# Performance work log

Hardware: AMD Instinct MI355X
Metric: run time of the kernel (lower is better)

Reference implementation:

```python
import jax, jax.numpy as jnp
import numpy as np

N, IN_DIM, OUT_DIM, HEADS = 4096, 256, 256, 8
D_HEAD = (OUT_DIM * HEADS) // HEADS  # = OUT_DIM per the torch code
HIDDEN = OUT_DIM * 4
LN_EPS = 1e-5


def setup_inputs() -> dict:
    key = jax.random.key(0)
    ks = jax.random.split(key, 8)
    s = 0.02
    return {
        "x": jax.random.normal(ks[0], (N, IN_DIM), jnp.float32),
        "Wq": jax.random.normal(ks[1], (OUT_DIM * HEADS, IN_DIM), jnp.float32) * s,
        "Wk": jax.random.normal(ks[2], (OUT_DIM * HEADS, IN_DIM), jnp.float32) * s,
        "Wv": jax.random.normal(ks[3], (OUT_DIM * HEADS, IN_DIM), jnp.float32) * s,
        "Wo": jax.random.normal(ks[4], (OUT_DIM, OUT_DIM * HEADS), jnp.float32) * s,
        "bo": jnp.zeros((OUT_DIM,), jnp.float32),
        "ln1_g": jnp.ones((IN_DIM,), jnp.float32),
        "ln1_b": jnp.zeros((IN_DIM,), jnp.float32),
        "ln2_g": jnp.ones((OUT_DIM,), jnp.float32),
        "ln2_b": jnp.zeros((OUT_DIM,), jnp.float32),
        "W1": jax.random.normal(ks[5], (HIDDEN, OUT_DIM), jnp.float32) * s,
        "b1": jnp.zeros((HIDDEN,), jnp.float32),
        "W2": jax.random.normal(ks[6], (OUT_DIM, HIDDEN), jnp.float32) * s,
        "b2": jnp.zeros((OUT_DIM,), jnp.float32),
    }


def _layernorm(x, g, b):
    mu = jnp.mean(x, axis=-1, keepdims=True)
    var = jnp.mean(jnp.square(x - mu), axis=-1, keepdims=True)
    return (x - mu) * jax.lax.rsqrt(var + LN_EPS) * g + b


def reference(x, Wq, Wk, Wv, Wo, bo, ln1_g, ln1_b, ln2_g, ln2_b, W1, b1, W2, b2):
    n = x.shape[0]
    h = _layernorm(x, ln1_g, ln1_b)
    # projections: F.linear(h, W) = h @ W.T, viewed as [N, H, d_head]
    Q = (h @ Wq.T).reshape(n, HEADS, D_HEAD)
    K = (h @ Wk.T).reshape(n, HEADS, D_HEAD)
    V = (h @ Wv.T).reshape(n, HEADS, D_HEAD)
    scores = jnp.einsum('nhd,mhd->nhm', Q, K) / jnp.sqrt(jnp.float32(D_HEAD))
    probs = jax.nn.softmax(scores, axis=-1)
    attn = jnp.einsum('nhm,mhd->nhd', probs, V).reshape(n, HEADS * D_HEAD)
    attn_out = attn @ Wo.T + bo
    x = x + attn_out  # proj_residual is Identity (in_dim == out_dim)
    h2 = _layernorm(x, ln2_g, ln2_b)
    ffn = jax.nn.gelu(h2 @ W1.T + b1, approximate=False) @ W2.T + b2
    return x + ffn
```

## Files before the change

kernel.cpp:

```cpp
#include <hip/hip_runtime.h>

typedef __attribute__((ext_vector_type(8))) short short8;
typedef __attribute__((ext_vector_type(4))) float f32x4;
typedef __attribute__((ext_vector_type(16))) float f32x16;
typedef __attribute__((ext_vector_type(8))) int i32x8;
typedef unsigned short u16;
typedef unsigned int u32;
typedef unsigned char u8;

#define DEVFN static __device__ __forceinline__

DEVFN u16 f2b(float f) {
  u32 u = __builtin_bit_cast(u32, f);
  u32 r = u + 0x7fffu + ((u >> 16) & 1u);
  return (u16)(r >> 16);
}

DEVFN float b2f(u16 b) {
  u32 u = ((u32)b) << 16;
  return __builtin_bit_cast(float, u);
}

DEVFN short8 ldfrag(const void* p) {
  return __builtin_bit_cast(short8, *(const uint4*)p);
}

#define MFMA16(a, b, c) __builtin_amdgcn_mfma_f32_16x16x32_bf16((a), (b), (c), 0, 0, 0)
#define MFMAS(a, b, c) __builtin_amdgcn_mfma_scale_f32_32x32x64_f8f6f4((a), (b), (c), 0, 0, 0, 127, 0, 127)
#define EXP2(x) __builtin_amdgcn_exp2f(x)

DEVFN i32x8 mk8(uint4 a, uint4 b) {
  return (i32x8){(int)a.x, (int)a.y, (int)a.z, (int)a.w, (int)b.x, (int)b.y, (int)b.z, (int)b.w};
}

DEVFN void llds16(const void* g, void* l) {
  __builtin_amdgcn_global_load_lds((const __attribute__((address_space(1))) void*)g,
                                   (__attribute__((address_space(3))) void*)l, 16, 0, 0);
}

DEVFN float gelu_exact(float v) {
  return 0.5f * v * (1.0f + erff(v * 0.70710678118654752f));
}

DEVFN int sigma(int d) {
  return (d & ~24) | ((d & 8) << 1) | ((d & 16) >> 1);
}

__global__ __launch_bounds__(256) void k_prep(const float* s0, const float* s1, const float* s2,
                                              const float* s3, const float* s4, const float* s5,
                                              u16* d0, u16* d1, u16* d2, u16* d3, u16* d4, u16* d5,
                                              const float* x, const float* g1, const float* be1,
                                              u16* hb) {
  const int y = blockIdx.y;
  if (y < 6) {
    int i = blockIdx.x * 256 + threadIdx.x;
    const float* s;
    u16* d;
    int n4;
    switch (y) {
      case 0: s = s0; d = d0; n4 = 131072; break;
      case 1: s = s1; d = d1; n4 = 131072; break;
      case 2: s = s2; d = d2; n4 = 131072; break;
      case 3: s = s3; d = d3; n4 = 131072; break;
      case 4: s = s4; d = d4; n4 = 65536; break;
      default: s = s5; d = d5; n4 = 65536; break;
    }
    if (i >= n4) return;
    float4 v = ((const float4*)s)[i];
    ushort4 o = { f2b(v.x), f2b(v.y), f2b(v.z), f2b(v.w) };
    ((ushort4*)d)[i] = o;
    return;
  }
  int row = blockIdx.x * 4 + (threadIdx.x >> 6);
  int l = threadIdx.x & 63;
  const float4 v = *(const float4*)(x + (size_t)row * 256 + l * 4);
  float s = v.x + v.y + v.z + v.w;
#pragma unroll
  for (int m = 1; m < 64; m <<= 1) s += __shfl_xor(s, m);
  float mu = s * (1.0f / 256.0f);
  float dx = v.x - mu, dy = v.y - mu, dz = v.z - mu, dw = v.w - mu;
  float q = dx * dx + dy * dy + dz * dz + dw * dw;
#pragma unroll
  for (int m = 1; m < 64; m <<= 1) q += __shfl_xor(q, m);
  float r = rsqrtf(q * (1.0f / 256.0f) + 1e-5f);
  float4 gv = *(const float4*)(g1 + l * 4);
  float4 bv = *(const float4*)(be1 + l * 4);
  ushort4 o = { f2b(dx * r * gv.x + bv.x), f2b(dy * r * gv.y + bv.y),
                f2b(dz * r * gv.z + bv.z), f2b(dw * r * gv.w + bv.w) };
  *(ushort4*)(hb + (size_t)row * 256 + l * 4) = o;
}

template <int EPI>
__global__ __launch_bounds__(256, 2) void k_gemm(const u16* __restrict__ A,
                                                 const u16* __restrict__ B,
                                                 void* __restrict__ out,
                                                 const float* __restrict__ bias,
                                                 int M, int N, int K) {
  __shared__ __attribute__((aligned(16))) u16 As[128 * 32];
  __shared__ __attribute__((aligned(16))) u16 Bs[128 * 32];
  const int t = threadIdx.x;
  const int w = t >> 6, l = t & 63, g = l >> 4, c = l & 15;
  const int wr = w >> 1, wc = w & 1;
  const int bm = blockIdx.y, bn = blockIdx.x;

  f32x4 acc[4][4] = {};
  int nk = K >> 5, kk0 = 0;
  if (EPI == 4) { nk = nk / gridDim.z; kk0 = blockIdx.z * nk; }

  const int srow = t >> 2;
  const int sj = t & 3;
  const char* Abase = (const char*)A;
  const char* Bbase = (const char*)B;

  for (int kk = kk0; kk < kk0 + nk; ++kk) {
    const size_t kb = (size_t)kk * 64;
    uint4 a0 = *(const uint4*)(Abase + ((size_t)(bm * 128 + srow) * K) * 2 + kb + sj * 16);
    uint4 a1 = *(const uint4*)(Abase + ((size_t)(bm * 128 + srow + 64) * K) * 2 + kb + sj * 16);
    uint4 b0 = *(const uint4*)(Bbase + ((size_t)(bn * 128 + srow) * K) * 2 + kb + sj * 16);
    uint4 b1 = *(const uint4*)(Bbase + ((size_t)(bn * 128 + srow + 64) * K) * 2 + kb + sj * 16);
    __syncthreads();
    const int sw0 = (sj * 16) ^ (((srow >> 1) & 3) << 4);
    const int sw1 = (sj * 16) ^ ((((srow + 64) >> 1) & 3) << 4);
    *(uint4*)((char*)As + srow * 64 + sw0) = a0;
    *(uint4*)((char*)As + (srow + 64) * 64 + sw1) = a1;
    *(uint4*)((char*)Bs + srow * 64 + sw0) = b0;
    *(uint4*)((char*)Bs + (srow + 64) * 64 + sw1) = b1;
    __syncthreads();
    short8 af[4], bfr[4];
#pragma unroll
    for (int m = 0; m < 4; ++m) {
      int row = wr * 64 + m * 16 + c;
      af[m] = ldfrag((const char*)As + row * 64 + ((g * 16) ^ (((row >> 1) & 3) << 4)));
    }
#pragma unroll
    for (int n = 0; n < 4; ++n) {
      int row = wc * 64 + n * 16 + c;
      bfr[n] = ldfrag((const char*)Bs + row * 64 + ((g * 16) ^ (((row >> 1) & 3) << 4)));
    }
#pragma unroll
    for (int m = 0; m < 4; ++m)
#pragma unroll
      for (int n = 0; n < 4; ++n) acc[m][n] = MFMA16(af[m], bfr[n], acc[m][n]);
  }

  const int row0 = bm * 128 + wr * 64 + 4 * g;
  const int col0 = bn * 128 + wc * 64 + c;
#pragma unroll
  for (int m = 0; m < 4; ++m) {
#pragma unroll
    for (int n = 0; n < 4; ++n) {
      const int row = row0 + m * 16;
      const int col = col0 + n * 16;
      if (EPI == 3) {
        float bc = bias[col];
#pragma unroll
        for (int rr = 0; rr < 4; ++rr)
          ((u16*)out)[(size_t)(row + rr) * N + col] = f2b(gelu_exact(acc[m][n][rr] + bc));
      } else {
        float* po = (float*)out + (size_t)blockIdx.z * M * N;
#pragma unroll
        for (int rr = 0; rr < 4; ++rr)
          po[(size_t)(row + rr) * N + col] = acc[m][n][rr];
      }
    }
  }
}

__global__ __launch_bounds__(256, 2) void k_gemm_wo(const u16* __restrict__ part,
                                                    const float* __restrict__ ml,
                                                    const u16* __restrict__ B,
                                                    float* __restrict__ out) {
  constexpr int M = 4096, N = 256, K = 2048;
  __shared__ __attribute__((aligned(16))) u16 As[128 * 32];
  __shared__ __attribute__((aligned(16))) u16 Bs[128 * 32];
  const int t = threadIdx.x;
  const int w = t >> 6, l = t & 63, g = l >> 4, c = l & 15;
  const int wr = w >> 1, wc = w & 1;
  const int bm = blockIdx.y, bn = blockIdx.x;
  const int nk = 16, kk0 = blockIdx.z * 16;
  const int h0 = kk0 >> 3;

  const int srow = t >> 2;
  const int sj = t & 3;
  const int r0 = bm * 128 + srow, r1 = r0 + 64;

  float wgt[4];
#pragma unroll
  for (int rr = 0; rr < 2; ++rr) {
    const int row = rr ? r1 : r0;
#pragma unroll
    for (int hh = 0; hh < 2; ++hh) {
      const int h = h0 + hh;
      float l0 = ml[(0 + h) * 4096 + row];
      float l1 = ml[(8 + h) * 4096 + row];
      wgt[rr * 2 + hh] = 1.0f / (l0 + l1);
    }
  }

  f32x4 acc[4][4] = {};
  const char* Pbase = (const char*)part;
  const char* Bbase = (const char*)B;
  const size_t PSTRIDE = (size_t)4096 * 2048 * 2;

  for (int kk = kk0; kk < kk0 + nk; ++kk) {
    const int hh = (kk >> 3) & 1;
    const size_t kb = (size_t)kk * 64;
    const size_t a0off = ((size_t)r0 * K) * 2 + kb + sj * 16;
    const size_t a1off = ((size_t)r1 * K) * 2 + kb + sj * 16;
    uint4 p00 = *(const uint4*)(Pbase + a0off);
    uint4 p01 = *(const uint4*)(Pbase + PSTRIDE + a0off);
    uint4 p10 = *(const uint4*)(Pbase + a1off);
    uint4 p11 = *(const uint4*)(Pbase + PSTRIDE + a1off);
    uint4 b0 = *(const uint4*)(Bbase + ((size_t)(bn * 128 + srow) * K) * 2 + kb + sj * 16);
    uint4 b1 = *(const uint4*)(Bbase + ((size_t)(bn * 128 + srow + 64) * K) * 2 + kb + sj * 16);

    float w0 = wgt[hh], w1 = wgt[2 + hh];
    uint4 a0, a1;
    {
      const u16* x0 = (const u16*)&p00;
      const u16* x1 = (const u16*)&p01;
      u16* o = (u16*)&a0;
#pragma unroll
      for (int j = 0; j < 8; ++j) o[j] = f2b((b2f(x0[j]) + b2f(x1[j])) * w0);
      const u16* y0 = (const u16*)&p10;
      const u16* y1 = (const u16*)&p11;
      u16* o1 = (u16*)&a1;
#pragma unroll
      for (int j = 0; j < 8; ++j) o1[j] = f2b((b2f(y0[j]) + b2f(y1[j])) * w1);
    }

    __syncthreads();
    const int sw0 = (sj * 16) ^ (((srow >> 1) & 3) << 4);
    const int sw1 = (sj * 16) ^ ((((srow + 64) >> 1) & 3) << 4);
    *(uint4*)((char*)As + srow * 64 + sw0) = a0;
    *(uint4*)((char*)As + (srow + 64) * 64 + sw1) = a1;
    *(uint4*)((char*)Bs + srow * 64 + sw0) = b0;
    *(uint4*)((char*)Bs + (srow + 64) * 64 + sw1) = b1;
    __syncthreads();
    short8 af[4], bfr[4];
#pragma unroll
    for (int m = 0; m < 4; ++m) {
      int row = wr * 64 + m * 16 + c;
      af[m] = ldfrag((const char*)As + row * 64 + ((g * 16) ^ (((row >> 1) & 3) << 4)));
    }
#pragma unroll
    for (int n = 0; n < 4; ++n) {
      int row = wc * 64 + n * 16 + c;
      bfr[n] = ldfrag((const char*)Bs + row * 64 + ((g * 16) ^ (((row >> 1) & 3) << 4)));
    }
#pragma unroll
    for (int m = 0; m < 4; ++m)
#pragma unroll
      for (int n = 0; n < 4; ++n) acc[m][n] = MFMA16(af[m], bfr[n], acc[m][n]);
  }

  const int row0 = bm * 128 + wr * 64 + 4 * g;
  const int col0 = bn * 128 + wc * 64 + c;
  float* po = out + (size_t)blockIdx.z * M * N;
#pragma unroll
  for (int m = 0; m < 4; ++m)
#pragma unroll
    for (int n = 0; n < 4; ++n)
#pragma unroll
      for (int rr = 0; rr < 4; ++rr)
        po[(size_t)(row0 + m * 16 + rr) * N + col0 + n * 16] = acc[m][n][rr];
}

__global__ __launch_bounds__(256, 2) void k_gemm_qkv(const u16* __restrict__ A,
                                                     const u16* __restrict__ Bq,
                                                     const u16* __restrict__ Bk,
                                                     const u16* __restrict__ Bv,
                                                     u8* __restrict__ Oq,
                                                     u8* __restrict__ Ok,
                                                     u8* __restrict__ Ov8) {
  constexpr int M = 4096, N = 2048, K = 256;
  __shared__ __attribute__((aligned(16))) u16 As[128 * 32];
  __shared__ __attribute__((aligned(16))) u16 Bs[128 * 32];
  const int t = threadIdx.x;
  const int w = t >> 6, l = t & 63, g = l >> 4, c = l & 15;
  const int wr = w >> 1, wc = w & 1;
  const int sel = blockIdx.x >> 4;
  const int bn = blockIdx.x & 15;
  const int bm = blockIdx.y;
  const u16* B = sel == 0 ? Bq : (sel == 1 ? Bk : Bv);

  f32x4 acc[4][4] = {};
  const int srow = t >> 2;
  const int sj = t & 3;
  const char* Abase = (const char*)A;
  const char* Bbase = (const char*)B;

  for (int kk = 0; kk < 8; ++kk) {
    const size_t kb = (size_t)kk * 64;
    uint4 a0 = *(const uint4*)(Abase + ((size_t)(bm * 128 + srow) * K) * 2 + kb + sj * 16);
    uint4 a1 = *(const uint4*)(Abase + ((size_t)(bm * 128 + srow + 64) * K) * 2 + kb + sj * 16);
    uint4 b0 = *(const uint4*)(Bbase + ((size_t)(bn * 128 + srow) * K) * 2 + kb + sj * 16);
    uint4 b1 = *(const uint4*)(Bbase + ((size_t)(bn * 128 + srow + 64) * K) * 2 + kb + sj * 16);
    __syncthreads();
    const int sw0 = (sj * 16) ^ (((srow >> 1) & 3) << 4);
    const int sw1 = (sj * 16) ^ ((((srow + 64) >> 1) & 3) << 4);
    *(uint4*)((char*)As + srow * 64 + sw0) = a0;
    *(uint4*)((char*)As + (srow + 64) * 64 + sw1) = a1;
    *(uint4*)((char*)Bs + srow * 64 + sw0) = b0;
    *(uint4*)((char*)Bs + (srow + 64) * 64 + sw1) = b1;
    __syncthreads();
    short8 af[4], bfr[4];
#pragma unroll
    for (int m = 0; m < 4; ++m) {
      int row = wr * 64 + m * 16 + c;
      af[m] = ldfrag((const char*)As + row * 64 + ((g * 16) ^ (((row >> 1) & 3) << 4)));
    }
#pragma unroll
    for (int n = 0; n < 4; ++n) {
      int row = wc * 64 + n * 16 + c;
      bfr[n] = ldfrag((const char*)Bs + row * 64 + ((g * 16) ^ (((row >> 1) & 3) << 4)));
    }
#pragma unroll
    for (int m = 0; m < 4; ++m)
#pragma unroll
      for (int n = 0; n < 4; ++n) acc[m][n] = MFMA16(af[m], bfr[n], acc[m][n]);
  }

  const int row0 = bm * 128 + wr * 64 + 4 * g;
  const int col0 = bn * 128 + wc * 64 + c;
  if (sel == 0) {
#pragma unroll
    for (int m = 0; m < 4; ++m) {
#pragma unroll
      for (int n = 0; n < 4; ++n) {
        const int col = col0 + n * 16;
        u32 lo = __builtin_amdgcn_cvt_pk_fp8_f32(acc[m][n][0], acc[m][n][1], 0, false);
        u32 hi2 = __builtin_amdgcn_cvt_pk_fp8_f32(acc[m][n][2], acc[m][n][3], 0, false);
        u32 quad = (lo & 0xffffu) | (hi2 << 16);
#pragma unroll
        for (int rr = 0; rr < 4; ++rr) {
          const int row = row0 + m * 16 + rr;
          Oq[(size_t)row * 2048 + col] = (u8)(quad >> (8 * rr));
        }
      }
    }
  } else if (sel == 1) {
#pragma unroll
    for (int m = 0; m < 4; ++m) {
#pragma unroll
      for (int n = 0; n < 4; ++n) {
        const int col = col0 + n * 16;
        const int d = col & 255, h = col >> 8;
        u32 lo = __builtin_amdgcn_cvt_pk_fp8_f32(acc[m][n][0], acc[m][n][1], 0, false);
        u32 hi2 = __builtin_amdgcn_cvt_pk_fp8_f32(acc[m][n][2], acc[m][n][3], 0, false);
        u32 quad = (lo & 0xffffu) | (hi2 << 16);
#pragma unroll
        for (int rr = 0; rr < 4; ++rr) {
          const int kv = row0 + m * 16 + rr;
          Ok[(size_t)h * 1048576 + (size_t)(kv >> 5) * 8192 + (d >> 6) * 2048 +
             (((d & 31) >> 4)) * 1024 + ((kv & 31) + 32 * ((d >> 5) & 1)) * 16 + (d & 15)] =
              (u8)(quad >> (8 * rr));
        }
      }
    }
  } else {
#pragma unroll
    for (int m = 0; m < 4; ++m)
#pragma unroll
      for (int n = 0; n < 4; ++n) {
        const int col = col0 + n * 16;
        const int d = col & 255, h = col >> 8;
        u32 q = __builtin_amdgcn_cvt_pk_fp8_f32(acc[m][n][0], acc[m][n][1], 0, false);
        q = __builtin_amdgcn_cvt_pk_fp8_f32(acc[m][n][2], acc[m][n][3], q, true);
        const int kv = row0 + m * 16;
        const int s = sigma(kv & 31);
        *(u32*)(Ov8 + (size_t)h * 1048576 + (size_t)(kv >> 6) * 16384 + (d >> 5) * 2048 +
                ((kv >> 5) & 1) * 1024 + ((d & 31) + 32 * (s >> 4)) * 16 + (s & 15)) = q;
      }
  }
}

__global__ __launch_bounds__(256) void k_red4(const float* __restrict__ p,
                                              const float* __restrict__ bias,
                                              const float* __restrict__ resid,
                                              float* __restrict__ out) {
  int i = blockIdx.x * 256 + threadIdx.x;
  const float4* p4 = (const float4*)p;
  float4 a = p4[i], b = p4[i + 262144], c = p4[i + 524288], d = p4[i + 786432];
  float4 r = ((const float4*)resid)[i];
  float4 bb = ((const float4*)bias)[i & 63];
  float4 o;
  o.x = a.x + b.x + c.x + d.x + r.x + bb.x;
  o.y = a.y + b.y + c.y + d.y + r.y + bb.y;
  o.z = a.z + b.z + c.z + d.z + r.z + bb.z;
  o.w = a.w + b.w + c.w + d.w + r.w + bb.w;
  ((float4*)out)[i] = o;
}

__global__ __launch_bounds__(256) void k_red4ln(const float* __restrict__ p,
                                                const float* __restrict__ bias,
                                                const float* __restrict__ resid,
                                                const float* __restrict__ g,
                                                const float* __restrict__ b,
                                                float* __restrict__ x2,
                                                u16* __restrict__ out) {
  int row = blockIdx.x * 4 + (threadIdx.x >> 6);
  int l = threadIdx.x & 63;
  int i = row * 64 + l;
  const float4* p4 = (const float4*)p;
  float4 a = p4[i], bq = p4[i + 262144], cq = p4[i + 524288], dq = p4[i + 786432];
  float4 r = ((const float4*)resid)[i];
  float4 bi = ((const float4*)bias)[l];
  float4 v;
  v.x = a.x + bq.x + cq.x + dq.x + r.x + bi.x;
  v.y = a.y + bq.y + cq.y + dq.y + r.y + bi.y;
  v.z = a.z + bq.z + cq.z + dq.z + r.z + bi.z;
  v.w = a.w + bq.w + cq.w + dq.w + r.w + bi.w;
  ((float4*)x2)[i] = v;
  float s = v.x + v.y + v.z + v.w;
#pragma unroll
  for (int m = 1; m < 64; m <<= 1) s += __shfl_xor(s, m);
  float mu = s * (1.0f / 256.0f);
  float dx = v.x - mu, dy = v.y - mu, dz = v.z - mu, dw = v.w - mu;
  float q = dx * dx + dy * dy + dz * dz + dw * dw;
#pragma unroll
  for (int m = 1; m < 64; m <<= 1) q += __shfl_xor(q, m);
  float rr = rsqrtf(q * (1.0f / 256.0f) + 1e-5f);
  float4 gv = *(const float4*)(g + l * 4);
  float4 bv = *(const float4*)(b + l * 4);
  ushort4 o = { f2b(dx * rr * gv.x + bv.x), f2b(dy * rr * gv.y + bv.y),
                f2b(dz * rr * gv.z + bv.z), f2b(dw * rr * gv.w + bv.w) };
  *(ushort4*)(out + (size_t)row * 256 + l * 4) = o;
}

__global__ __launch_bounds__(256, 2) void k_attn(const u8* __restrict__ Q8,
                                                 const u8* __restrict__ K8,
                                                 const u8* __restrict__ V8,
                                                 u16* __restrict__ part,
                                                 float* __restrict__ ml) {
  __shared__ __attribute__((aligned(16))) char smem[49152];
  const int t = threadIdx.x;
  const int w = t >> 6, l = t & 63;
  const int q31 = l & 31, hi = l >> 5;
  const int head = blockIdx.x, qb = blockIdx.y, sp = blockIdx.z;
  const int cbase = sp * 64;
  const float C2 = 0.0625f * 1.44269504f;
  const float MC = 16.0f * C2;

  i32x8 qv[4];
  {
    const u8* qp = Q8 + (size_t)(qb * 128 + w * 32 + q31) * 2048 + head * 256 + hi * 32;
#pragma unroll
    for (int m = 0; m < 4; ++m)
      qv[m] = mk8(*(const uint4*)(qp + m * 64), *(const uint4*)(qp + m * 64 + 16));
  }

  f32x16 o[8] = {};
  float lsum = 0.0f;

  const u8* Kc = K8 + (size_t)head * 1048576;
  const u8* Vc = V8 + (size_t)head * 1048576;

  auto stageK = [&](int cc) {
    char* kd = smem + (cc & 1) * 8192;
    const u8* src = Kc + (size_t)(cbase + cc) * 8192;
#pragma unroll
    for (int ii = 0; ii < 2; ++ii) {
      const int inst = w * 2 + ii;
      llds16(src + inst * 1024 + l * 16, kd + inst * 1024);
    }
  };
  auto stageV = [&](int pp) {
    char* vd = smem + 16384 + (pp & 1) * 16384;
    const u8* src = Vc + (size_t)(sp * 32 + pp) * 16384;
#pragma unroll
    for (int ii = 0; ii < 4; ++ii) {
      const int inst = w * 4 + ii;
      llds16(src + inst * 1024 + l * 16, vd + inst * 1024);
    }
  };

  auto qkchunk = [&](int c, u32 pq[4]) {
    const char* kd = smem + (c & 1) * 8192;
    f32x16 s = {};
    __builtin_amdgcn_s_setprio(1);
#pragma unroll
    for (int m = 0; m < 4; ++m) {
      uint4 k0 = *(const uint4*)(kd + m * 2048 + l * 16);
      uint4 k1 = *(const uint4*)(kd + m * 2048 + 1024 + l * 16);
      s = MFMAS(mk8(k0, k1), qv[m], s);
    }
    __builtin_amdgcn_s_setprio(0);
    float p[16];
#pragma unroll
    for (int i = 0; i < 16; ++i) p[i] = EXP2(fmaf(s[i], C2, -MC));
    float r8[8];
#pragma unroll
    for (int i = 0; i < 8; ++i) r8[i] = p[i] + p[i + 8];
#pragma unroll
    for (int i = 0; i < 4; ++i) r8[i] += r8[i + 4];
    float rs = (r8[0] + r8[1]) + (r8[2] + r8[3]);
    rs += __shfl_xor(rs, 32);
    lsum += rs;
    u32 a0 = __builtin_amdgcn_cvt_pk_fp8_f32(p[0], p[1], 0, false);
    a0 = __builtin_amdgcn_cvt_pk_fp8_f32(p[2], p[3], a0, true);
    u32 a1 = __builtin_amdgcn_cvt_pk_fp8_f32(p[4], p[5], 0, false);
    a1 = __builtin_amdgcn_cvt_pk_fp8_f32(p[6], p[7], a1, true);
    u32 a2 = __builtin_amdgcn_cvt_pk_fp8_f32(p[8], p[9], 0, false);
    a2 = __builtin_amdgcn_cvt_pk_fp8_f32(p[10], p[11], a2, true);
    u32 a3 = __builtin_amdgcn_cvt_pk_fp8_f32(p[12], p[13], 0, false);
    a3 = __builtin_amdgcn_cvt_pk_fp8_f32(p[14], p[15], a3, true);
    asm("v_permlane32_swap_b32 %0, %1" : "+v"(a0), "+v"(a1));
    asm("v_permlane32_swap_b32 %0, %1" : "+v"(a2), "+v"(a3));
    pq[0] = a0; pq[1] = a1; pq[2] = a2; pq[3] = a3;
  };

  stageK(0);
  stageV(0);
  for (int cp = 0; cp < 32; ++cp) {
    const int c0 = 2 * cp;
    asm volatile("s_waitcnt vmcnt(4)" ::: "memory");
    __builtin_amdgcn_s_barrier();
    __builtin_amdgcn_sched_barrier(0);
    stageK(c0 + 1);
    u32 pe[4];
    qkchunk(c0, pe);

    asm volatile("s_waitcnt vmcnt(0)" ::: "memory");
    __builtin_amdgcn_s_barrier();
    __builtin_amdgcn_sched_barrier(0);
    if (cp < 31) {
      stageK(c0 + 2);
      stageV(cp + 1);
    }
    u32 po[4];
    qkchunk(c0 + 1, po);

    i32x8 a8 = {(int)pe[0], (int)pe[1], (int)pe[2], (int)pe[3],
                (int)po[0], (int)po[1], (int)po[2], (int)po[3]};
    const char* vd = smem + 16384 + (cp & 1) * 16384;
    __builtin_amdgcn_s_setprio(1);
#pragma unroll
    for (int dt = 0; dt < 8; ++dt) {
      uint4 v0 = *(const uint4*)(vd + dt * 2048 + l * 16);
      uint4 v1 = *(const uint4*)(vd + dt * 2048 + 1024 + l * 16);
      o[dt] = MFMAS(a8, mk8(v0, v1), o[dt]);
    }
    __builtin_amdgcn_s_setprio(0);
  }

  u16* pb = part + (size_t)sp * 4096 * 2048;
#pragma unroll
  for (int i = 0; i < 16; ++i) {
    const int r = (i & 3) + 8 * (i >> 2) + 4 * hi;
    const size_t qg = (size_t)(qb * 128 + w * 32 + r);
#pragma unroll
    for (int dt = 0; dt < 8; ++dt)
      pb[qg * 2048 + head * 256 + dt * 32 + q31] = f2b(o[dt][i]);
  }
  if (hi == 0) {
    const int qg = qb * 128 + w * 32 + q31;
    ml[(sp * 8 + head) * 4096 + qg] = lsum;
  }
}

extern "C" void kernel_launch(void* const* d_in, const int* in_sizes, int n_in,
                              void* d_out, int out_size, void* d_ws, size_t ws_size,
                              hipStream_t stream) {
  const float* x   = (const float*)d_in[0];
  const float* Wq  = (const float*)d_in[1];
  const float* Wk  = (const float*)d_in[2];
  const float* Wv  = (const float*)d_in[3];
  const float* Wo  = (const float*)d_in[4];
  const float* bo  = (const float*)d_in[5];
  const float* g1  = (const float*)d_in[6];
  const float* be1 = (const float*)d_in[7];
  const float* g2  = (const float*)d_in[8];
  const float* be2 = (const float*)d_in[9];
  const float* W1  = (const float*)d_in[10];
  const float* b1  = (const float*)d_in[11];
  const float* W2  = (const float*)d_in[12];
  const float* b2  = (const float*)d_in[13];

  char* ws = (char*)d_ws;
  size_t off = 0;
  auto alloc = [&](size_t n) {
    char* p = ws + off;
    off = (off + n + 255) & ~(size_t)255;
    return p;
  };
  u16* hb    = (u16*)alloc(4096 * 256 * 2);
  u16* Wqb   = (u16*)alloc(2048 * 256 * 2);
  u16* Wkb   = (u16*)alloc(2048 * 256 * 2);
  u16* Wvb   = (u16*)alloc(2048 * 256 * 2);
  u16* Wob   = (u16*)alloc(256 * 2048 * 2);
  u16* W1b   = (u16*)alloc(1024 * 256 * 2);
  u16* W2b   = (u16*)alloc(256 * 1024 * 2);
  u8*  Qb8   = (u8*)alloc((size_t)4096 * 2048);
  u8*  Kb8   = (u8*)alloc((size_t)4096 * 2048);
  u8*  Vb8   = (u8*)alloc((size_t)2048 * 4096);
  u16* attnb = (u16*)alloc((size_t)2 * 4096 * 2048 * 2);
  float* mlb = (float*)alloc(16 * 4096 * 4);
  float* x2  = (float*)alloc(4096 * 256 * 4);
  u16* h2b   = (u16*)alloc(4096 * 256 * 2);
  u16* ffn1  = (u16*)alloc((size_t)4096 * 1024 * 2);
  float* pbuf = (float*)Qb8;

  k_prep<<<dim3(1024, 7), 256, 0, stream>>>(Wq, Wk, Wv, Wo, W1, W2,
                                            Wqb, Wkb, Wvb, Wob, W1b, W2b,
                                            x, g1, be1, hb);

  k_gemm_qkv<<<dim3(48, 32), 256, 0, stream>>>(hb, Wqb, Wkb, Wvb, Qb8, Kb8, Vb8);

  k_attn<<<dim3(8, 32, 2), 256, 0, stream>>>(Qb8, Kb8, Vb8, attnb, mlb);

  k_gemm_wo<<<dim3(2, 32, 4), 256, 0, stream>>>(attnb, mlb, Wob, pbuf);
  k_red4ln<<<1024, 256, 0, stream>>>(pbuf, bo, x, g2, be2, x2, h2b);
  k_gemm<3><<<dim3(8, 32), 256, 0, stream>>>(h2b, W1b, ffn1, b1, 4096, 1024, 256);
  k_gemm<4><<<dim3(2, 32, 4), 256, 0, stream>>>(ffn1, W2b, pbuf, nullptr, 4096, 256, 1024);
  k_red4<<<1024, 256, 0, stream>>>(pbuf, b2, x2, (float*)d_out);
}
```

Baseline: 160.5 us.

## Run QKV projection in FP8 with pre-tiled operands loaded straight into LDS

LayerNorm output and the Wq/Wk/Wv weights are now quantised to FP8 in the prep kernel. The weights are scaled by 16, with an exponent scale in the MFMA to undo it. Both operands are written in a tiled layout that matches the 32x32x64 scaled MFMA fragments. The QKV GEMM loads the whole K=256 tile into LDS with global_load_lds in one shot, with no K-loop of staging and barriers, and uses the FP8 MFMA. This halves operand bytes and raises matrix throughput, but adds quantisation error to the inputs of the Q/K/V projections.

```diff
diff --git a/kernel.cpp b/kernel.cpp
--- a/kernel.cpp
+++ b/kernel.cpp
@@ -27,7 +27,9 @@
 
 #define MFMA16(a, b, c) __builtin_amdgcn_mfma_f32_16x16x32_bf16((a), (b), (c), 0, 0, 0)
 #define MFMAS(a, b, c) __builtin_amdgcn_mfma_scale_f32_32x32x64_f8f6f4((a), (b), (c), 0, 0, 0, 127, 0, 127)
+#define MFMASW(a, b, c) __builtin_amdgcn_mfma_scale_f32_32x32x64_f8f6f4((a), (b), (c), 0, 0, 0, 127, 0, 123)
 #define EXP2(x) __builtin_amdgcn_exp2f(x)
+#define CVT8(a, b, o, hi) __builtin_amdgcn_cvt_pk_fp8_f32((a), (b), (o), (hi))
 
 DEVFN i32x8 mk8(uint4 a, uint4 b) {
   return (i32x8){(int)a.x, (int)a.y, (int)a.z, (int)a.w, (int)b.x, (int)b.y, (int)b.z, (int)b.w};
@@ -46,24 +48,38 @@
   return (d & ~24) | ((d & 8) << 1) | ((d & 16) >> 1);
 }
 
-__global__ __launch_bounds__(256) void k_prep(const float* s0, const float* s1, const float* s2,
-                                              const float* s3, const float* s4, const float* s5,
-                                              u16* d0, u16* d1, u16* d2, u16* d3, u16* d4, u16* d5,
+DEVFN size_t c8off(int row, int k) {
+  return (size_t)(row >> 5) * 8192 + (k >> 6) * 2048 + ((row & 31) + 32 * ((k >> 5) & 1)) * 32 + (k & 31);
+}
+
+__global__ __launch_bounds__(256) void k_prep(const float* Wq, const float* Wk, const float* Wv,
+                                              const float* Wo, const float* W1, const float* W2,
+                                              u8* Wq8, u8* Wk8, u8* Wv8,
+                                              u16* Wob, u16* W1b, u16* W2b,
                                               const float* x, const float* g1, const float* be1,
-                                              u16* hb) {
+                                              u8* h8c) {
   const int y = blockIdx.y;
+  if (y < 3) {
+    int i = blockIdx.x * 256 + threadIdx.x;
+    if (i >= 131072) return;
+    const float* s = y == 0 ? Wq : (y == 1 ? Wk : Wv);
+    u8* d = y == 0 ? Wq8 : (y == 1 ? Wk8 : Wv8);
+    float4 v = ((const float4*)s)[i];
+    const int col = i >> 6, k = (i & 63) * 4;
+    u32 q = CVT8(v.x * 16.0f, v.y * 16.0f, 0, false);
+    q = CVT8(v.z * 16.0f, v.w * 16.0f, q, true);
+    *(u32*)(d + c8off(col, k)) = q;
+    return;
+  }
   if (y < 6) {
     int i = blockIdx.x * 256 + threadIdx.x;
     const float* s;
     u16* d;
     int n4;
     switch (y) {
-      case 0: s = s0; d = d0; n4 = 131072; break;
-      case 1: s = s1; d = d1; n4 = 131072; break;
-      case 2: s = s2; d = d2; n4 = 131072; break;
-      case 3: s = s3; d = d3; n4 = 131072; break;
-      case 4: s = s4; d = d4; n4 = 65536; break;
-      default: s = s5; d = d5; n4 = 65536; break;
+      case 3: s = Wo; d = Wob; n4 = 131072; break;
+      case 4: s = W1; d = W1b; n4 = 65536; break;
+      default: s = W2; d = W2b; n4 = 65536; break;
     }
     if (i >= n4) return;
     float4 v = ((const float4*)s)[i];
@@ -85,9 +101,9 @@
   float r = rsqrtf(q * (1.0f / 256.0f) + 1e-5f);
   float4 gv = *(const float4*)(g1 + l * 4);
   float4 bv = *(const float4*)(be1 + l * 4);
-  ushort4 o = { f2b(dx * r * gv.x + bv.x), f2b(dy * r * gv.y + bv.y),
-                f2b(dz * r * gv.z + bv.z), f2b(dw * r * gv.w + bv.w) };
-  *(ushort4*)(hb + (size_t)row * 256 + l * 4) = o;
+  u32 pk = CVT8(dx * r * gv.x + bv.x, dy * r * gv.y + bv.y, 0, false);
+  pk = CVT8(dz * r * gv.z + bv.z, dw * r * gv.w + bv.w, pk, true);
+  *(u32*)(h8c + c8off(row, l * 4)) = pk;
 }
 
 template <int EPI>
@@ -266,112 +282,88 @@
         po[(size_t)(row0 + m * 16 + rr) * N + col0 + n * 16] = acc[m][n][rr];
 }
 
-__global__ __launch_bounds__(256, 2) void k_gemm_qkv(const u16* __restrict__ A,
-                                                     const u16* __restrict__ Bq,
-                                                     const u16* __restrict__ Bk,
-                                                     const u16* __restrict__ Bv,
+__global__ __launch_bounds__(256, 2) void k_gemm_qkv(const u8* __restrict__ h8c,
+                                                     const u8* __restrict__ Wq8,
+                                                     const u8* __restrict__ Wk8,
+                                                     const u8* __restrict__ Wv8,
                                                      u8* __restrict__ Oq,
                                                      u8* __restrict__ Ok,
                                                      u8* __restrict__ Ov8) {
-  constexpr int M = 4096, N = 2048, K = 256;
-  __shared__ __attribute__((aligned(16))) u16 As[128 * 32];
-  __shared__ __attribute__((aligned(16))) u16 Bs[128 * 32];
+  __shared__ __attribute__((aligned(16))) char As[32768];
+  __shared__ __attribute__((aligned(16))) char Bs[32768];
   const int t = threadIdx.x;
-  const int w = t >> 6, l = t & 63, g = l >> 4, c = l & 15;
+  const int w = t >> 6, l = t & 63;
+  const int q31 = l & 31, hi = l >> 5;
   const int wr = w >> 1, wc = w & 1;
   const int sel = blockIdx.x >> 4;
   const int bn = blockIdx.x & 15;
   const int bm = blockIdx.y;
-  const u16* B = sel == 0 ? Bq : (sel == 1 ? Bk : Bv);
-
-  f32x4 acc[4][4] = {};
-  const int srow = t >> 2;
-  const int sj = t & 3;
-  const char* Abase = (const char*)A;
-  const char* Bbase = (const char*)B;
-
-  for (int kk = 0; kk < 8; ++kk) {
-    const size_t kb = (size_t)kk * 64;
-    uint4 a0 = *(const uint4*)(Abase + ((size_t)(bm * 128 + srow) * K) * 2 + kb + sj * 16);
-    uint4 a1 = *(const uint4*)(Abase + ((size_t)(bm * 128 + srow + 64) * K) * 2 + kb + sj * 16);
-    uint4 b0 = *(const uint4*)(Bbase + ((size_t)(bn * 128 + srow) * K) * 2 + kb + sj * 16);
-    uint4 b1 = *(const uint4*)(Bbase + ((size_t)(bn * 128 + srow + 64) * K) * 2 + kb + sj * 16);
-    __syncthreads();
-    const int sw0 = (sj * 16) ^ (((srow >> 1) & 3) << 4);
-    const int sw1 = (sj * 16) ^ ((((srow + 64) >> 1) & 3) << 4);
-    *(uint4*)((char*)As + srow * 64 + sw0) = a0;
-    *(uint4*)((char*)As + (srow + 64) * 64 + sw1) = a1;
-    *(uint4*)((char*)Bs + srow * 64 + sw0) = b0;
-    *(uint4*)((char*)Bs + (srow + 64) * 64 + sw1) = b1;
-    __syncthreads();
-    short8 af[4], bfr[4];
-#pragma unroll
-    for (int m = 0; m < 4; ++m) {
-      int row = wr * 64 + m * 16 + c;
-      af[m] = ldfrag((const char*)As + row * 64 + ((g * 16) ^ (((row >> 1) & 3) << 4)));
-    }
-#pragma unroll
-    for (int n = 0; n < 4; ++n) {
-      int row = wc * 64 + n * 16 + c;
-      bfr[n] = ldfrag((const char*)Bs + row * 64 + ((g * 16) ^ (((row >> 1) & 3) << 4)));
-    }
-#pragma unroll
-    for (int m = 0; m < 4; ++m)
-#pragma unroll
-      for (int n = 0; n < 4; ++n) acc[m][n] = MFMA16(af[m], bfr[n], acc[m][n]);
-  }
-
-  const int row0 = bm * 128 + wr * 64 + 4 * g;
-  const int col0 = bn * 128 + wc * 64 + c;
-  if (sel == 0) {
-#pragma unroll
-    for (int m = 0; m < 4; ++m) {
-#pragma unroll
-      for (int n = 0; n < 4; ++n) {
-        const int col = col0 + n * 16;
-        u32 lo = __builtin_amdgcn_cvt_pk_fp8_f32(acc[m][n][0], acc[m][n][1], 0, false);
-        u32 hi2 = __builtin_amdgcn_cvt_pk_fp8_f32(acc[m][n][2], acc[m][n][3], 0, false);
-        u32 quad = (lo & 0xffffu) | (hi2 << 16);
-#pragma unroll
-        for (int rr = 0; rr < 4; ++rr) {
-          const int row = row0 + m * 16 + rr;
-          Oq[(size_t)row * 2048 + col] = (u8)(quad >> (8 * rr));
+  const u8* B = sel == 0 ? Wq8 : (sel == 1 ? Wk8 : Wv8);
+
+#pragma unroll
+  for (int ii = 0; ii < 8; ++ii) {
+    const int inst = w * 8 + ii;
+    llds16(h8c + (size_t)bm * 32768 + inst * 1024 + l * 16, As + inst * 1024);
+  }
+#pragma unroll
+  for (int ii = 0; ii < 8; ++ii) {
+    const int inst = w * 8 + ii;
+    llds16(B + (size_t)bn * 32768 + inst * 1024 + l * 16, Bs + inst * 1024);
+  }
+  asm volatile("s_waitcnt vmcnt(0)" ::: "memory");
+  __builtin_amdgcn_s_barrier();
+
+  f32x16 acc[2][2] = {};
+#pragma unroll
+  for (int ks = 0; ks < 4; ++ks) {
+    i32x8 af[2], bf8[2];
+#pragma unroll
+    for (int m = 0; m < 2; ++m) {
+      const char* p = As + ((wr * 2 + m) * 4 + ks) * 2048 + l * 32;
+      af[m] = mk8(*(const uint4*)p, *(const uint4*)(p + 16));
+    }
+#pragma unroll
+    for (int n = 0; n < 2; ++n) {
+      const char* p = Bs + ((wc * 2 + n) * 4 + ks) * 2048 + l * 32;
+      bf8[n] = mk8(*(const uint4*)p, *(const uint4*)(p + 16));
+    }
+#pragma unroll
+    for (int m = 0; m < 2; ++m)
+#pragma unroll
+      for (int n = 0; n < 2; ++n) acc[m][n] = MFMASW(af[m], bf8[n], acc[m][n]);
+  }
+
+#pragma unroll
+  for (int m = 0; m < 2; ++m) {
+#pragma unroll
+    for (int n = 0; n < 2; ++n) {
+      const int col = bn * 128 + wc * 64 + n * 32 + q31;
+      const int rbase = bm * 128 + wr * 64 + m * 32 + 4 * hi;
+      const int d = col & 255, h = col >> 8;
+#pragma unroll
+      for (int j = 0; j < 4; ++j) {
+        const int kv0 = rbase + 8 * j;
+        u32 q = CVT8(acc[m][n][4 * j], acc[m][n][4 * j + 1], 0, false);
+        q = CVT8(acc[m][n][4 * j + 2], acc[m][n][4 * j + 3], q, true);
+        if (sel == 0) {
+#pragma unroll
+          for (int e = 0; e < 4; ++e)
+            Oq[(size_t)(kv0 + e) * 2048 + col] = (u8)(q >> (8 * e));
+        } else if (sel == 1) {
+#pragma unroll
+          for (int e = 0; e < 4; ++e) {
+            const int kv = kv0 + e;
+            Ok[(size_t)h * 1048576 + (size_t)(kv >> 5) * 8192 + (d >> 6) * 2048 +
+               (((d & 31) >> 4)) * 1024 + ((kv & 31) + 32 * ((d >> 5) & 1)) * 16 + (d & 15)] =
+                (u8)(q >> (8 * e));
+          }
+        } else {
+          const int s = sigma(kv0 & 31);
+          *(u32*)(Ov8 + (size_t)h * 1048576 + (size_t)(kv0 >> 6) * 16384 + (d >> 5) * 2048 +
+                  ((kv0 >> 5) & 1) * 1024 + ((d & 31) + 32 * (s >> 4)) * 16 + (s & 15)) = q;
         }
       }
     }
-  } else if (sel == 1) {
-#pragma unroll
-    for (int m = 0; m < 4; ++m) {
-#pragma unroll
-      for (int n = 0; n < 4; ++n) {
-        const int col = col0 + n * 16;
-        const int d = col & 255, h = col >> 8;
-        u32 lo = __builtin_amdgcn_cvt_pk_fp8_f32(acc[m][n][0], acc[m][n][1], 0, false);
-        u32 hi2 = __builtin_amdgcn_cvt_pk_fp8_f32(acc[m][n][2], acc[m][n][3], 0, false);
-        u32 quad = (lo & 0xffffu) | (hi2 << 16);
-#pragma unroll
-        for (int rr = 0; rr < 4; ++rr) {
-          const int kv = row0 + m * 16 + rr;
-          Ok[(size_t)h * 1048576 + (size_t)(kv >> 5) * 8192 + (d >> 6) * 2048 +
-             (((d & 31) >> 4)) * 1024 + ((kv & 31) + 32 * ((d >> 5) & 1)) * 16 + (d & 15)] =
-              (u8)(quad >> (8 * rr));
-        }
-      }
-    }
-  } else {
-#pragma unroll
-    for (int m = 0; m < 4; ++m)
-#pragma unroll
-      for (int n = 0; n < 4; ++n) {
-        const int col = col0 + n * 16;
-        const int d = col & 255, h = col >> 8;
-        u32 q = __builtin_amdgcn_cvt_pk_fp8_f32(acc[m][n][0], acc[m][n][1], 0, false);
-        q = __builtin_amdgcn_cvt_pk_fp8_f32(acc[m][n][2], acc[m][n][3], q, true);
-        const int kv = row0 + m * 16;
-        const int s = sigma(kv & 31);
-        *(u32*)(Ov8 + (size_t)h * 1048576 + (size_t)(kv >> 6) * 16384 + (d >> 5) * 2048 +
-                ((kv >> 5) & 1) * 1024 + ((d & 31) + 32 * (s >> 4)) * 16 + (s & 15)) = q;
-      }
   }
 }
 
@@ -497,14 +489,14 @@
     float rs = (r8[0] + r8[1]) + (r8[2] + r8[3]);
     rs += __shfl_xor(rs, 32);
     lsum += rs;
-    u32 a0 = __builtin_amdgcn_cvt_pk_fp8_f32(p[0], p[1], 0, false);
-    a0 = __builtin_amdgcn_cvt_pk_fp8_f32(p[2], p[3], a0, true);
-    u32 a1 = __builtin_amdgcn_cvt_pk_fp8_f32(p[4], p[5], 0, false);
-    a1 = __builtin_amdgcn_cvt_pk_fp8_f32(p[6], p[7], a1, true);
-    u32 a2 = __builtin_amdgcn_cvt_pk_fp8_f32(p[8], p[9], 0, false);
-    a2 = __builtin_amdgcn_cvt_pk_fp8_f32(p[10], p[11], a2, true);
-    u32 a3 = __builtin_amdgcn_cvt_pk_fp8_f32(p[12], p[13], 0, false);
-    a3 = __builtin_amdgcn_cvt_pk_fp8_f32(p[14], p[15], a3, true);
+    u32 a0 = CVT8(p[0], p[1], 0, false);
+    a0 = CVT8(p[2], p[3], a0, true);
+    u32 a1 = CVT8(p[4], p[5], 0, false);
+    a1 = CVT8(p[6], p[7], a1, true);
+    u32 a2 = CVT8(p[8], p[9], 0, false);
+    a2 = CVT8(p[10], p[11], a2, true);
+    u32 a3 = CVT8(p[12], p[13], 0, false);
+    a3 = CVT8(p[14], p[15], a3, true);
     asm("v_permlane32_swap_b32 %0, %1" : "+v"(a0), "+v"(a1));
     asm("v_permlane32_swap_b32 %0, %1" : "+v"(a2), "+v"(a3));
     pq[0] = a0; pq[1] = a1; pq[2] = a2; pq[3] = a3;
@@ -584,10 +576,10 @@
     off = (off + n + 255) & ~(size_t)255;
     return p;
   };
-  u16* hb    = (u16*)alloc(4096 * 256 * 2);
-  u16* Wqb   = (u16*)alloc(2048 * 256 * 2);
-  u16* Wkb   = (u16*)alloc(2048 * 256 * 2);
-  u16* Wvb   = (u16*)alloc(2048 * 256 * 2);
+  u8*  h8c   = (u8*)alloc(4096 * 256);
+  u8*  Wq8   = (u8*)alloc(2048 * 256);
+  u8*  Wk8   = (u8*)alloc(2048 * 256);
+  u8*  Wv8   = (u8*)alloc(2048 * 256);
   u16* Wob   = (u16*)alloc(256 * 2048 * 2);
   u16* W1b   = (u16*)alloc(1024 * 256 * 2);
   u16* W2b   = (u16*)alloc(256 * 1024 * 2);
@@ -602,10 +594,10 @@
   float* pbuf = (float*)Qb8;
 
   k_prep<<<dim3(1024, 7), 256, 0, stream>>>(Wq, Wk, Wv, Wo, W1, W2,
-                                            Wqb, Wkb, Wvb, Wob, W1b, W2b,
-                                            x, g1, be1, hb);
-
-  k_gemm_qkv<<<dim3(48, 32), 256, 0, stream>>>(hb, Wqb, Wkb, Wvb, Qb8, Kb8, Vb8);
+                                            Wq8, Wk8, Wv8, Wob, W1b, W2b,
+                                            x, g1, be1, h8c);
+
+  k_gemm_qkv<<<dim3(48, 32), 256, 0, stream>>>(h8c, Wq8, Wk8, Wv8, Qb8, Kb8, Vb8);
 
   k_attn<<<dim3(8, 32, 2), 256, 0, stream>>>(Qb8, Kb8, Vb8, attnb, mlb);
 
```

After: 151.5 us. -5.6%, faster.
